# Performance work log

Measured on AMD Instinct MI355X. Metric: run time of the kernel, lower is better.

Reference implementation:

```python
import jax, jax.numpy as jnp
import numpy as np

D_MODEL = 1024
N_HEADS = 16
D_K = D_MODEL // N_HEADS
B, S = 8, 1024
EPS = 1e-8


def setup_inputs() -> dict:
    key = jax.random.key(0)
    ks = jax.random.split(key, 6)
    scale = 1.0 / np.sqrt(D_MODEL)
    return {
        "Q_in": jax.random.normal(ks[0], (B, S, D_MODEL), jnp.float32),
        "mask": jax.random.randint(ks[1], (B, 1, S, S), 0, 2, jnp.int32),
        "Wq": jax.random.normal(ks[2], (D_MODEL, D_MODEL), jnp.float32) * scale,
        "bq": jnp.zeros((D_MODEL,), jnp.float32),
        "Wk": jax.random.normal(ks[3], (D_MODEL, D_MODEL), jnp.float32) * scale,
        "bk": jnp.zeros((D_MODEL,), jnp.float32),
        "Wv": jax.random.normal(ks[4], (D_MODEL, D_MODEL), jnp.float32) * scale,
        "bv": jnp.zeros((D_MODEL,), jnp.float32),
        "Wo": jax.random.normal(ks[5], (D_MODEL, D_MODEL), jnp.float32) * scale,
        "bo": jnp.zeros((D_MODEL,), jnp.float32),
    }


def reference(Q_in, mask, Wq, bq, Wk, bk, Wv, bv, Wo, bo):
    # QKV projections: [B,S,D] -> [B,H,S,d_k]
    def split_heads(x):
        return x.reshape(B, S, N_HEADS, D_K).transpose(0, 2, 1, 3)

    Q = split_heads(Q_in @ Wq + bq)
    K = split_heads(Q_in @ Wk + bk)
    V = split_heads(Q_in @ Wv + bv)

    # scaled scores [B,H,S,S], standard softmax
    scores = jnp.einsum("bhqd,bhkd->bhqk", Q, K) / jnp.sqrt(
        jnp.asarray(D_K, jnp.float32))
    scores = jax.nn.softmax(scores, axis=-1)
    # non-standard: multiplicative mask AFTER softmax, then row renorm
    scores = scores * mask.astype(scores.dtype)
    attn = scores / (jnp.sum(scores, axis=-1, keepdims=True) + EPS)

    context = jnp.einsum("bhqk,bhkd->bhqd", attn, V)
    context = context.transpose(0, 2, 1, 3).reshape(B, S, D_MODEL)
    return context @ Wo + bo
```

## Files before the change

### kernel.cpp

```cpp
#include <hip/hip_runtime.h>
#include <hip/hip_bf16.h>
#include <stdint.h>

typedef __attribute__((ext_vector_type(4))) float f32x4;
typedef __attribute__((ext_vector_type(8))) __bf16 bf16x8;
typedef unsigned short u16;
typedef unsigned int u32;

#define NH 16
#define DKK 64

__device__ __forceinline__ u16 f2bf(float f) {
    u32 u = __builtin_bit_cast(u32, f);
    u32 r = (u + 0x7fffu + ((u >> 16) & 1u)) >> 16;
    return (u16)r;
}

__device__ __forceinline__ void gload16(const void* g, void* l) {
    __builtin_amdgcn_global_load_lds((const __attribute__((address_space(1))) void*)g,
                                     (__attribute__((address_space(3))) void*)l, 16, 0, 0);
}

__global__ __launch_bounds__(256) void k_convert_x(const float* __restrict__ x,
                                                   u16* __restrict__ xb) {
    int i = blockIdx.x * 256 + threadIdx.x;
    const float4* p = (const float4*)x + (size_t)i * 2;
    float4 a = p[0], b = p[1];
    union { u16 h[8]; uint4 q; } o;
    o.h[0] = f2bf(a.x); o.h[1] = f2bf(a.y); o.h[2] = f2bf(a.z); o.h[3] = f2bf(a.w);
    o.h[4] = f2bf(b.x); o.h[5] = f2bf(b.y); o.h[6] = f2bf(b.z); o.h[7] = f2bf(b.w);
    ((uint4*)xb)[i] = o.q;
}

__global__ __launch_bounds__(256) void k_convert_w(const float* __restrict__ wq,
                                                   const float* __restrict__ wk,
                                                   const float* __restrict__ wv,
                                                   const float* __restrict__ wo,
                                                   u16* __restrict__ wt) {
    int z = blockIdx.z;
    const float* w = (z == 0) ? wq : (z == 1) ? wk : (z == 2) ? wv : wo;
    __shared__ float t[32][33];
    int tx = threadIdx.x & 31, ty = threadIdx.x >> 5;
    int n0 = blockIdx.x * 32, k0 = blockIdx.y * 32;
    for (int rr = 0; rr < 4; ++rr)
        t[ty + rr * 8][tx] = w[(size_t)(k0 + ty + rr * 8) * 1024 + n0 + tx];
    __syncthreads();
    for (int rr = 0; rr < 4; ++rr) {
        int n = n0 + ty + rr * 8;
        wt[((size_t)z * 1024 + n) * 1024 + k0 + tx] = f2bf(t[tx][ty + rr * 8]);
    }
}

template <int MODE>
__global__ __launch_bounds__(256) void k_gemm(const u16* __restrict__ A,
                                              const u16* __restrict__ Bt,
                                              const float* __restrict__ b0,
                                              const float* __restrict__ b1,
                                              const float* __restrict__ b2,
                                              u16* __restrict__ q_out,
                                              u16* __restrict__ k_out,
                                              u16* __restrict__ v_out,
                                              float* __restrict__ out) {
    __shared__ u16 As[128 * 32];
    __shared__ u16 Bs[128 * 32];
    int tid = threadIdx.x;
    int wv = tid >> 6, lane = tid & 63;
    int r = lane & 15, g = lane >> 4;
    int wr = wv >> 1, wc = wv & 1;
    int m0 = blockIdx.x * 128, n0 = blockIdx.y * 128;
    f32x4 acc[4][4] = {};
    for (int kt = 0; kt < 1024; kt += 32) {
        __syncthreads();
        for (int i = 0; i < 2; ++i) {
            int e = i * 256 + tid;
            int row = e >> 2, c8 = (e & 3) * 8;
            const u16* ga = A + (size_t)(m0 + row) * 1024 + kt + c8;
            const u16* gb = Bt + (size_t)(n0 + row) * 1024 + kt + c8;
            gload16(ga, As + (size_t)(i * 256 + wv * 64) * 8);
            gload16(gb, Bs + (size_t)(i * 256 + wv * 64) * 8);
        }
        __syncthreads();
        bf16x8 aF[4], bF[4];
        for (int m = 0; m < 4; ++m) aF[m] = *(const bf16x8*)&As[(wr * 64 + m * 16 + r) * 32 + g * 8];
        for (int n = 0; n < 4; ++n) bF[n] = *(const bf16x8*)&Bs[(wc * 64 + n * 16 + r) * 32 + g * 8];
        for (int m = 0; m < 4; ++m)
            for (int n = 0; n < 4; ++n)
                acc[m][n] = __builtin_amdgcn_mfma_f32_16x16x32_bf16(aF[m], bF[n], acc[m][n], 0, 0, 0);
    }
    for (int m = 0; m < 4; ++m) {
        int rowb = m0 + wr * 64 + m * 16 + 4 * g;
        for (int n = 0; n < 4; ++n) {
            int col = n0 + wc * 64 + n * 16 + r;
            if (MODE == 0) {
                int w = col >> 10, cn = col & 1023;
                const float* bp = (w == 0) ? b0 : (w == 1) ? b1 : b2;
                u16* dst = (w == 0) ? q_out : (w == 1) ? k_out : v_out;
                float sc = (w == 0) ? 0.125f : 1.0f;
                int h = cn >> 6, d = cn & 63;
                float bias = bp[cn];
                for (int i = 0; i < 4; ++i) {
                    int row = rowb + i;
                    int b = row >> 10, s = row & 1023;
                    float v = (acc[m][n][i] + bias) * sc;
                    dst[((size_t)(b * NH + h) * 1024 + s) * 64 + d] = f2bf(v);
                }
            } else {
                float bias = b0[col];
                for (int i = 0; i < 4; ++i) {
                    int row = rowb + i;
                    out[(size_t)row * 1024 + col] = acc[m][n][i] + bias;
                }
            }
        }
    }
}

__global__ __launch_bounds__(256) void k_transpose_v(const u16* __restrict__ vb,
                                                     u16* __restrict__ vt) {
    __shared__ u16 t[64][72];
    int bh = blockIdx.y, s0 = blockIdx.x * 64;
    int tid = threadIdx.x;
    for (int i = 0; i < 2; ++i) {
        int e = i * 256 + tid;
        int row = e >> 3, ch = (e & 7) * 8;
        uint4 v = *(const uint4*)(vb + ((size_t)bh * 1024 + s0 + row) * 64 + ch);
        *(uint4*)&t[row][ch] = v;
    }
    __syncthreads();
    for (int i = 0; i < 2; ++i) {
        int e = i * 256 + tid;
        int d = e >> 3, ch = (e & 7) * 8;
        union { u16 h[8]; uint4 q; } o;
        for (int j = 0; j < 8; ++j) o.h[j] = t[ch + j][d];
        *(uint4*)(vt + ((size_t)bh * 64 + d) * 1024 + s0 + ch) = o.q;
    }
}

__global__ __launch_bounds__(256) void k_attn(const u16* __restrict__ qb,
                                              const u16* __restrict__ kb,
                                              const u16* __restrict__ vt,
                                              const int* __restrict__ mask,
                                              u16* __restrict__ ctx) {
    __shared__ u16 K_lds[64 * 64];
    __shared__ u16 V_lds[64 * 64];
    __shared__ u16 P_lds[4 * 16 * 64];
    int tid = threadIdx.x, wv = tid >> 6, lane = tid & 63;
    int r = lane & 15, g = lane >> 4;
    int q0 = blockIdx.x * 64, bh = blockIdx.y;
    int b = bh >> 4, h = bh & 15;

    bf16x8 aq[2];
    {
        const u16* qp = qb + ((size_t)bh * 1024 + q0 + wv * 16 + r) * 64 + g * 8;
        aq[0] = *(const bf16x8*)qp;
        aq[1] = *(const bf16x8*)(qp + 32);
    }
    float Zr[4] = {0.f, 0.f, 0.f, 0.f}, Zm[4] = {0.f, 0.f, 0.f, 0.f};
    f32x4 of[4] = {};

    int swzr = ((r >> 2) & 3) | ((r & 1) << 2);

    for (int kt = 0; kt < 1024; kt += 64) {
        __syncthreads();
        for (int i2 = 0; i2 < 2; ++i2) {
            int e = i2 * 256 + tid;
            int row = e >> 3, c = e & 7;
            int cs = (c ^ (row & 7)) * 8;
            const u16* gk = kb + ((size_t)bh * 1024 + kt + row) * 64 + cs;
            const u16* gv = vt + ((size_t)bh * 64 + row) * 1024 + kt + cs;
            gload16(gk, K_lds + (size_t)(i2 * 256 + wv * 64) * 8);
            gload16(gv, V_lds + (size_t)(i2 * 256 + wv * 64) * 8);
        }
        __syncthreads();
        f32x4 sf[4];
        for (int nf = 0; nf < 4; ++nf) {
            int rowk = (nf * 16 + r) * 64;
            bf16x8 bk0 = *(const bf16x8*)&K_lds[rowk + ((g ^ (r & 7)) << 3)];
            bf16x8 bk1 = *(const bf16x8*)&K_lds[rowk + (((g + 4) ^ (r & 7)) << 3)];
            f32x4 z = {0.f, 0.f, 0.f, 0.f};
            z = __builtin_amdgcn_mfma_f32_16x16x32_bf16(aq[0], bk0, z, 0, 0, 0);
            z = __builtin_amdgcn_mfma_f32_16x16x32_bf16(aq[1], bk1, z, 0, 0, 0);
            sf[nf] = z;
        }
        for (int i = 0; i < 4; ++i) {
            int prow = 4 * g + i;
            int qrow = q0 + wv * 16 + prow;
            const int* mrow = mask + ((size_t)b * 1024 + qrow) * 1024 + kt;
            int swzw = ((prow >> 2) & 3) | ((prow & 1) << 2);
            u16* pbase = P_lds + wv * 1024 + prow * 64;
            for (int nf = 0; nf < 4; ++nf) {
                int pcol = nf * 16 + r;
                float e = __expf(sf[nf][i]);
                Zr[i] += e;
                float em = mrow[pcol] ? e : 0.0f;
                Zm[i] += em;
                pbase[(((pcol >> 3) ^ swzw) << 3) + (pcol & 7)] = f2bf(em);
            }
        }
        __syncthreads();
        for (int kk = 0; kk < 2; ++kk) {
            bf16x8 ap = *(const bf16x8*)&P_lds[wv * 1024 + r * 64 + (((4 * kk + g) ^ swzr) << 3)];
            for (int nf = 0; nf < 4; ++nf) {
                bf16x8 bv = *(const bf16x8*)&V_lds[(nf * 16 + r) * 64 + (((4 * kk + g) ^ (r & 7)) << 3)];
                of[nf] = __builtin_amdgcn_mfma_f32_16x16x32_bf16(ap, bv, of[nf], 0, 0, 0);
            }
        }
    }
    for (int i = 0; i < 4; ++i) {
        float z = Zr[i], zm = Zm[i];
        z += __shfl_xor(z, 1); z += __shfl_xor(z, 2); z += __shfl_xor(z, 4); z += __shfl_xor(z, 8);
        zm += __shfl_xor(zm, 1); zm += __shfl_xor(zm, 2); zm += __shfl_xor(zm, 4); zm += __shfl_xor(zm, 8);
        float inv = 1.0f / (zm + 1e-8f * z);
        int qrow = q0 + wv * 16 + 4 * g + i;
        u16* crow = ctx + ((size_t)(b * 1024 + qrow)) * 1024 + h * 64;
        for (int nf = 0; nf < 4; ++nf)
            crow[nf * 16 + r] = f2bf(of[nf][i] * inv);
    }
}

extern "C" void kernel_launch(void* const* d_in, const int* in_sizes, int n_in,
                              void* d_out, int out_size, void* d_ws, size_t ws_size,
                              hipStream_t stream) {
    const float* Q_in = (const float*)d_in[0];
    const int*   mask = (const int*)d_in[1];
    const float* Wq = (const float*)d_in[2];
    const float* bq = (const float*)d_in[3];
    const float* Wk = (const float*)d_in[4];
    const float* bk = (const float*)d_in[5];
    const float* Wv = (const float*)d_in[6];
    const float* bv = (const float*)d_in[7];
    const float* Wo = (const float*)d_in[8];
    const float* bo = (const float*)d_in[9];

    char* ws = (char*)d_ws;
    u16* Xb = (u16*)(ws);
    u16* Wt = (u16*)(ws + 16777216);
    u16* Qb = (u16*)(ws + 25165824);
    u16* Kb = (u16*)(ws + 41943040);
    u16* Vb = (u16*)(ws + 58720256);
    u16* Vt = (u16*)(ws + 75497472);
    u16* Ctx = Vb;

    k_convert_x<<<4096, 256, 0, stream>>>(Q_in, Xb);
    k_convert_w<<<dim3(32, 32, 4), 256, 0, stream>>>(Wq, Wk, Wv, Wo, Wt);
    k_gemm<0><<<dim3(64, 24), 256, 0, stream>>>(Xb, Wt, bq, bk, bv, Qb, Kb, Vb, nullptr);
    k_transpose_v<<<dim3(16, 128), 256, 0, stream>>>(Vb, Vt);
    k_attn<<<dim3(16, 128), 256, 0, stream>>>(Qb, Kb, Vt, mask, Ctx);
    k_gemm<1><<<dim3(64, 8), 256, 0, stream>>>(Ctx, Wt + (size_t)3 * 1024 * 1024,
                                               bo, nullptr, nullptr,
                                               nullptr, nullptr, nullptr, (float*)d_out);
}
```

Measured before the change: 194.6 us.

## Pack mask to bitmask, double-buffer K/V, widen attention tiles to 256 queries

New measurement: 321.9 us. 65.4% more time.

```diff
diff --git a/kernel.cpp b/kernel.cpp
--- a/kernel.cpp
+++ b/kernel.cpp
@@ -6,6 +6,7 @@
 typedef __attribute__((ext_vector_type(8))) __bf16 bf16x8;
 typedef unsigned short u16;
 typedef unsigned int u32;
+typedef unsigned long long u64;
 
 #define NH 16
 #define DKK 64
@@ -14,6 +15,11 @@
     u32 u = __builtin_bit_cast(u32, f);
     u32 r = (u + 0x7fffu + ((u >> 16) & 1u)) >> 16;
     return (u16)r;
+}
+
+__device__ __forceinline__ u16 cvt_bf(float f) {
+    __hip_bfloat16 h = __float2bfloat16(f);
+    return *reinterpret_cast<u16*>(&h);
 }
 
 __device__ __forceinline__ void gload16(const void* g, void* l) {
@@ -48,6 +54,17 @@
     for (int rr = 0; rr < 4; ++rr) {
         int n = n0 + ty + rr * 8;
         wt[((size_t)z * 1024 + n) * 1024 + k0 + tx] = f2bf(t[tx][ty + rr * 8]);
+    }
+}
+
+__global__ __launch_bounds__(256) void k_maskpack(const int* __restrict__ mask,
+                                                  u64* __restrict__ mb) {
+    int wid = (blockIdx.x * 256 + threadIdx.x) >> 6;
+    int lane = threadIdx.x & 63;
+    for (int c = wid; c < 8 * 1024 * 16; c += 8192) {
+        int m = mask[(size_t)c * 64 + lane];
+        u64 bits = __ballot(m != 0);
+        if (lane == 0) mb[c] = bits;
     }
 }
 
@@ -136,85 +153,107 @@
     }
 }
 
-__global__ __launch_bounds__(256) void k_attn(const u16* __restrict__ qb,
-                                              const u16* __restrict__ kb,
-                                              const u16* __restrict__ vt,
-                                              const int* __restrict__ mask,
-                                              u16* __restrict__ ctx) {
-    __shared__ u16 K_lds[64 * 64];
-    __shared__ u16 V_lds[64 * 64];
-    __shared__ u16 P_lds[4 * 16 * 64];
+__global__ __launch_bounds__(512, 4) void k_attn(const u16* __restrict__ qb,
+                                                 const u16* __restrict__ kb,
+                                                 const u16* __restrict__ vt,
+                                                 const u64* __restrict__ mbits,
+                                                 u16* __restrict__ ctx) {
+    __shared__ u16 Kd[2][64 * 64];
+    __shared__ u16 Vd[2][64 * 64];
+    __shared__ u16 Pd[8][32 * 64];
     int tid = threadIdx.x, wv = tid >> 6, lane = tid & 63;
     int r = lane & 15, g = lane >> 4;
-    int q0 = blockIdx.x * 64, bh = blockIdx.y;
+
+    int lin = blockIdx.y * 4 + blockIdx.x;
+    int w = (lin & 7) * 64 + (lin >> 3);
+    int bh = w >> 2, xt = w & 3;
+    int q0 = xt * 256;
     int b = bh >> 4, h = bh & 15;
 
-    bf16x8 aq[2];
-    {
-        const u16* qp = qb + ((size_t)bh * 1024 + q0 + wv * 16 + r) * 64 + g * 8;
-        aq[0] = *(const bf16x8*)qp;
-        aq[1] = *(const bf16x8*)(qp + 32);
-    }
-    float Zr[4] = {0.f, 0.f, 0.f, 0.f}, Zm[4] = {0.f, 0.f, 0.f, 0.f};
-    f32x4 of[4] = {};
-
-    int swzr = ((r >> 2) & 3) | ((r & 1) << 2);
-
-    for (int kt = 0; kt < 1024; kt += 64) {
-        __syncthreads();
-        for (int i2 = 0; i2 < 2; ++i2) {
-            int e = i2 * 256 + tid;
-            int row = e >> 3, c = e & 7;
-            int cs = (c ^ (row & 7)) * 8;
-            const u16* gk = kb + ((size_t)bh * 1024 + kt + row) * 64 + cs;
-            const u16* gv = vt + ((size_t)bh * 64 + row) * 1024 + kt + cs;
-            gload16(gk, K_lds + (size_t)(i2 * 256 + wv * 64) * 8);
-            gload16(gv, V_lds + (size_t)(i2 * 256 + wv * 64) * 8);
-        }
-        __syncthreads();
-        f32x4 sf[4];
+    int srow = tid >> 3, sc = tid & 7;
+    int scs = (sc ^ (srow & 7)) * 8;
+    const u16* kbase = kb + ((size_t)bh * 1024 + srow) * 64 + scs;
+    const u16* vbase = vt + ((size_t)bh * 64 + srow) * 1024 + scs;
+
+    bf16x8 aq[2][2];
+    for (int qf = 0; qf < 2; ++qf) {
+        const u16* qp = qb + ((size_t)bh * 1024 + q0 + wv * 32 + qf * 16 + r) * 64 + g * 8;
+        aq[qf][0] = *(const bf16x8*)qp;
+        aq[qf][1] = *(const bf16x8*)(qp + 32);
+    }
+    float Zm[2][4] = {};
+    f32x4 of[2][4] = {};
+    u16* Pw = Pd[wv];
+
+    gload16(kbase, Kd[0] + tid * 8);
+    gload16(vbase + 0, Vd[0] + tid * 8);
+    __syncthreads();
+
+    for (int t = 0; t < 16; ++t) {
+        int cur = t & 1;
+        if (t < 15) {
+            int ktn = (t + 1) * 64;
+            gload16(kbase + (size_t)ktn * 64, Kd[cur ^ 1] + tid * 8);
+            gload16(vbase + ktn, Vd[cur ^ 1] + tid * 8);
+        }
+        const u16* K = Kd[cur];
+        const u16* V = Vd[cur];
+        int kt = t * 64;
+
+        bf16x8 bk0[4], bk1[4];
         for (int nf = 0; nf < 4; ++nf) {
             int rowk = (nf * 16 + r) * 64;
-            bf16x8 bk0 = *(const bf16x8*)&K_lds[rowk + ((g ^ (r & 7)) << 3)];
-            bf16x8 bk1 = *(const bf16x8*)&K_lds[rowk + (((g + 4) ^ (r & 7)) << 3)];
-            f32x4 z = {0.f, 0.f, 0.f, 0.f};
-            z = __builtin_amdgcn_mfma_f32_16x16x32_bf16(aq[0], bk0, z, 0, 0, 0);
-            z = __builtin_amdgcn_mfma_f32_16x16x32_bf16(aq[1], bk1, z, 0, 0, 0);
-            sf[nf] = z;
-        }
+            bk0[nf] = *(const bf16x8*)&K[rowk + ((g ^ (r & 7)) << 3)];
+            bk1[nf] = *(const bf16x8*)&K[rowk + (((g + 4) ^ (r & 7)) << 3)];
+        }
+        for (int qf = 0; qf < 2; ++qf) {
+            f32x4 sf[4];
+            for (int nf = 0; nf < 4; ++nf) {
+                f32x4 z = {0.f, 0.f, 0.f, 0.f};
+                z = __builtin_amdgcn_mfma_f32_16x16x32_bf16(aq[qf][0], bk0[nf], z, 0, 0, 0);
+                z = __builtin_amdgcn_mfma_f32_16x16x32_bf16(aq[qf][1], bk1[nf], z, 0, 0, 0);
+                sf[nf] = z;
+            }
+            for (int i = 0; i < 4; ++i) {
+                int prow = qf * 16 + 4 * g + i;
+                u64 mb = mbits[((size_t)b * 1024 + q0 + wv * 32 + prow) * 16 + t];
+                u64 mbr = mb >> r;
+                u16* pbase = Pw + prow * 64;
+                int sw = prow & 7;
+                float zm = 0.f;
+                for (int nf = 0; nf < 4; ++nf) {
+                    float e = __expf(sf[nf][i]);
+                    float em = ((mbr >> (nf * 16)) & 1) ? e : 0.0f;
+                    zm += em;
+                    pbase[(((2 * nf + (r >> 3)) ^ sw) << 3) + (r & 7)] = cvt_bf(em);
+                }
+                Zm[qf][i] += zm;
+            }
+        }
+        for (int kk = 0; kk < 2; ++kk) {
+            bf16x8 bvv[4];
+            for (int nf = 0; nf < 4; ++nf)
+                bvv[nf] = *(const bf16x8*)&V[(nf * 16 + r) * 64 + (((kk * 4 + g) ^ (r & 7)) << 3)];
+            for (int qf = 0; qf < 2; ++qf) {
+                bf16x8 ap = *(const bf16x8*)&Pw[(qf * 16 + r) * 64 + (((kk * 4 + g) ^ (r & 7)) << 3)];
+                for (int nf = 0; nf < 4; ++nf)
+                    of[qf][nf] = __builtin_amdgcn_mfma_f32_16x16x32_bf16(ap, bvv[nf], of[qf][nf], 0, 0, 0);
+            }
+        }
+        __syncthreads();
+    }
+
+    for (int qf = 0; qf < 2; ++qf) {
         for (int i = 0; i < 4; ++i) {
-            int prow = 4 * g + i;
-            int qrow = q0 + wv * 16 + prow;
-            const int* mrow = mask + ((size_t)b * 1024 + qrow) * 1024 + kt;
-            int swzw = ((prow >> 2) & 3) | ((prow & 1) << 2);
-            u16* pbase = P_lds + wv * 1024 + prow * 64;
-            for (int nf = 0; nf < 4; ++nf) {
-                int pcol = nf * 16 + r;
-                float e = __expf(sf[nf][i]);
-                Zr[i] += e;
-                float em = mrow[pcol] ? e : 0.0f;
-                Zm[i] += em;
-                pbase[(((pcol >> 3) ^ swzw) << 3) + (pcol & 7)] = f2bf(em);
-            }
-        }
-        __syncthreads();
-        for (int kk = 0; kk < 2; ++kk) {
-            bf16x8 ap = *(const bf16x8*)&P_lds[wv * 1024 + r * 64 + (((4 * kk + g) ^ swzr) << 3)];
-            for (int nf = 0; nf < 4; ++nf) {
-                bf16x8 bv = *(const bf16x8*)&V_lds[(nf * 16 + r) * 64 + (((4 * kk + g) ^ (r & 7)) << 3)];
-                of[nf] = __builtin_amdgcn_mfma_f32_16x16x32_bf16(ap, bv, of[nf], 0, 0, 0);
-            }
-        }
-    }
-    for (int i = 0; i < 4; ++i) {
-        float z = Zr[i], zm = Zm[i];
-        z += __shfl_xor(z, 1); z += __shfl_xor(z, 2); z += __shfl_xor(z, 4); z += __shfl_xor(z, 8);
-        zm += __shfl_xor(zm, 1); zm += __shfl_xor(zm, 2); zm += __shfl_xor(zm, 4); zm += __shfl_xor(zm, 8);
-        float inv = 1.0f / (zm + 1e-8f * z);
-        int qrow = q0 + wv * 16 + 4 * g + i;
-        u16* crow = ctx + ((size_t)(b * 1024 + qrow)) * 1024 + h * 64;
-        for (int nf = 0; nf < 4; ++nf)
-            crow[nf * 16 + r] = f2bf(of[nf][i] * inv);
+            float zm = Zm[qf][i];
+            zm += __shfl_xor(zm, 1); zm += __shfl_xor(zm, 2);
+            zm += __shfl_xor(zm, 4); zm += __shfl_xor(zm, 8);
+            float inv = 1.0f / zm;
+            int qrow = q0 + wv * 32 + qf * 16 + 4 * g + i;
+            u16* crow = ctx + ((size_t)(b * 1024 + qrow)) * 1024 + h * 64;
+            for (int nf = 0; nf < 4; ++nf)
+                crow[nf * 16 + r] = cvt_bf(of[qf][nf][i] * inv);
+        }
     }
 }
 
@@ -239,13 +278,15 @@
     u16* Kb = (u16*)(ws + 41943040);
     u16* Vb = (u16*)(ws + 58720256);
     u16* Vt = (u16*)(ws + 75497472);
+    u64* Mb = (u64*)(ws + 92274688);
     u16* Ctx = Vb;
 
     k_convert_x<<<4096, 256, 0, stream>>>(Q_in, Xb);
     k_convert_w<<<dim3(32, 32, 4), 256, 0, stream>>>(Wq, Wk, Wv, Wo, Wt);
+    k_maskpack<<<2048, 256, 0, stream>>>(mask, Mb);
     k_gemm<0><<<dim3(64, 24), 256, 0, stream>>>(Xb, Wt, bq, bk, bv, Qb, Kb, Vb, nullptr);
     k_transpose_v<<<dim3(16, 128), 256, 0, stream>>>(Vb, Vt);
-    k_attn<<<dim3(16, 128), 256, 0, stream>>>(Qb, Kb, Vt, mask, Ctx);
+    k_attn<<<dim3(4, 128), 512, 0, stream>>>(Qb, Kb, Vt, Mb, Ctx);
     k_gemm<1><<<dim3(64, 8), 256, 0, stream>>>(Ctx, Wt + (size_t)3 * 1024 * 1024,
                                                bo, nullptr, nullptr,
                                                nullptr, nullptr, nullptr, (float*)d_out);
```
